# Performance work log

Measured on AMD Instinct MI355X. Metric: run time of the kernel, lower is better.

Reference implementation:

```python
import jax, jax.numpy as jnp
import numpy as np
from jax import lax

TAU = 2.0
V_TH = 1.0
ALPHA = 4.0   # spikingjelly surrogate.Sigmoid default
BN_EPS = 1e-5
HEADS = 8


def lif(x):
    """Multi-step LIF neuron (tau=2, v_reset=0, hard reset, detach_reset).
    x: [T, ...] -> spikes [T, ...]. Forward is Heaviside; sigmoid surrogate
    is wired in via straight-through for the bwd variant."""
    def step(v, xt):
        v = v + (xt - v) / TAU                      # charge
        sg = jax.nn.sigmoid(ALPHA * (v - V_TH))     # surrogate
        hard = (v >= V_TH).astype(x.dtype)
        spike = sg + lax.stop_gradient(hard - sg)   # fwd: hard, bwd: sigmoid'
        v = v * (1.0 - lax.stop_gradient(spike))    # detached hard reset to 0
        return v, spike
    _, s = lax.scan(step, jnp.zeros_like(x[0]), x)
    return s


def conv1x1_bn(x, w, g, b, m, var, bias=None):
    # x: [N, C, H, W]; 1x1 conv == channel matmul, then eval-mode BN
    y = jnp.einsum('nchw,dc->ndhw', x, w)
    if bias is not None:
        y = y + bias[None, :, None, None]
    scale = g / jnp.sqrt(var + BN_EPS)
    shift = b - m * scale
    return y * scale[None, :, None, None] + shift[None, :, None, None]


def to_heads(x, T, B, C, H, W):
    # [T,B,C,H,W] -> [T,B,heads,N,hd]
    N = H * W
    hd = C // HEADS
    x = x.reshape(T, B, C, N).transpose(0, 1, 3, 2)          # [T,B,N,C]
    return x.reshape(T, B, N, HEADS, hd).transpose(0, 1, 3, 2, 4)


def _forward(x, q_w, q_bn_g, q_bn_b, q_bn_m, q_bn_v,
             k_w, k_bn_g, k_bn_b, k_bn_m, k_bn_v,
             v_w, v_bn_g, v_bn_b, v_bn_m, v_bn_v,
             out_w, out_b, out_bn_g, out_bn_b, out_bn_m, out_bn_v):
    T, B, C, H, W = x.shape
    N = H * W
    identity = x

    xs = lif(x)                                  # shortcut_lif
    x_qkv = xs.reshape(T * B, C, H, W)

    q = lif(conv1x1_bn(x_qkv, q_w, q_bn_g, q_bn_b, q_bn_m, q_bn_v).reshape(T, B, C, H, W))
    k = lif(conv1x1_bn(x_qkv, k_w, k_bn_g, k_bn_b, k_bn_m, k_bn_v).reshape(T, B, C, H, W))
    v = lif(conv1x1_bn(x_qkv, v_w, v_bn_g, v_bn_b, v_bn_m, v_bn_v).reshape(T, B, C, H, W))

    qh = to_heads(q, T, B, C, H, W)              # [T,B,h,N,hd]
    kh = to_heads(k, T, B, C, H, W)
    vh = to_heads(v, T, B, C, H, W)

    kv = jnp.sum(kh * vh, axis=-2, keepdims=True)   # [T,B,h,1,hd]
    kv = lif(kv)                                    # talking_heads_proj_lif
    y = qh * kv                                     # [T,B,h,N,hd]

    # [T,B,h,N,hd] -> transpose(3,4) -> [T,B,h,hd,N] -> [T,B,C,H,W]
    y = y.transpose(0, 1, 2, 4, 3).reshape(T, B, C, H, W)
    y = conv1x1_bn(y.reshape(T * B, C, H, W), out_w, out_bn_g, out_bn_b,
                   out_bn_m, out_bn_v, bias=out_b).reshape(T, B, C, H, W)
    return y + identity, vh


def setup_inputs() -> dict:
    key = jax.random.key(0)
    ks = jax.random.split(key, 6)
    T, B, C, H, W = 4, 32, 512, 14, 14
    inp = {
        'x': jax.random.normal(ks[0], (T, B, C, H, W), dtype=jnp.float32),
        'q_w': jax.random.normal(ks[1], (C, C), dtype=jnp.float32) * 0.05,
        'k_w': jax.random.normal(ks[2], (C, C), dtype=jnp.float32) * 0.05,
        'v_w': jax.random.normal(ks[3], (C, C), dtype=jnp.float32) * 0.05,
        'out_w': jax.random.normal(ks[4], (C, C), dtype=jnp.float32) * 0.05,
        'out_b': jnp.zeros((C,), dtype=jnp.float32),
    }
    for p in ('q', 'k', 'v', 'out'):
        inp[f'{p}_bn_g'] = jnp.ones((C,), dtype=jnp.float32)
        inp[f'{p}_bn_b'] = jnp.zeros((C,), dtype=jnp.float32)
        inp[f'{p}_bn_m'] = jnp.zeros((C,), dtype=jnp.float32)
        inp[f'{p}_bn_v'] = jnp.ones((C,), dtype=jnp.float32)
    return inp


def reference(x, q_w, q_bn_g, q_bn_b, q_bn_m, q_bn_v,
              k_w, k_bn_g, k_bn_b, k_bn_m, k_bn_v,
              v_w, v_bn_g, v_bn_b, v_bn_m, v_bn_v,
              out_w, out_b, out_bn_g, out_bn_b, out_bn_m, out_bn_v):
    return _forward(x, q_w, q_bn_g, q_bn_b, q_bn_m, q_bn_v,
                    k_w, k_bn_g, k_bn_b, k_bn_m, k_bn_v,
                    v_w, v_bn_g, v_bn_b, v_bn_m, v_bn_v,
                    out_w, out_b, out_bn_g, out_bn_b, out_bn_m, out_bn_v)
```

## Files before the change

### kernel.cpp

```cpp
#include <hip/hip_runtime.h>
#include <math.h>

#define T_   4
#define B_   32
#define C_   512
#define N_   196
#define TB_  128
#define M_   25088
#define BNP_ 6272
#define OUT1_ 12845056

typedef unsigned short ushort_t;
typedef __attribute__((ext_vector_type(8)))  __bf16 bf16x8;
typedef __attribute__((ext_vector_type(16))) float  f32x16;

__device__ __forceinline__ ushort_t f2bf(float f) {
    unsigned int u = __float_as_uint(f);
    u = u + 0x7FFFu + ((u >> 16) & 1u);
    return (ushort_t)(u >> 16);
}
__device__ __forceinline__ float bf2f(ushort_t h) {
    return __uint_as_float(((unsigned int)h) << 16);
}

#define GL2LDS(gp, lp) \
    __builtin_amdgcn_global_load_lds((const __attribute__((address_space(1))) void*)(gp), \
                                     (__attribute__((address_space(3))) void*)(lp), 16, 0, 0)

__global__ __launch_bounds__(256)
void prep_lifx_kernel(
    const float* __restrict__ qw, const float* __restrict__ kw,
    const float* __restrict__ vw, const float* __restrict__ ow,
    const float* __restrict__ qg, const float* __restrict__ qb, const float* __restrict__ qm, const float* __restrict__ qv,
    const float* __restrict__ kg, const float* __restrict__ kb, const float* __restrict__ km, const float* __restrict__ kvr,
    const float* __restrict__ vg, const float* __restrict__ vb, const float* __restrict__ vm, const float* __restrict__ vv,
    const float* __restrict__ og, const float* __restrict__ ob, const float* __restrict__ om, const float* __restrict__ ov,
    const float* __restrict__ obias,
    ushort_t* __restrict__ wsplit, ushort_t* __restrict__ osplit,
    float* __restrict__ scale_qkv, float* __restrict__ shift_qkv,
    float* __restrict__ scale_o,   float* __restrict__ shift_o,
    float* __restrict__ kvpart,
    const float* __restrict__ x, ushort_t* __restrict__ xs)
{
    __shared__ ushort_t tile[64 * 66];
    const int bid = blockIdx.x;
    const int tid = threadIdx.x;

    if (bid < 3072) {
        int i = bid * 256 + tid;
        int d = i >> 9, c = i & 511;
        const float* src = (d < 512) ? qw : (d < 1024) ? kw : vw;
        float wv = src[(d & 511) * 512 + c];
        ushort_t h = f2bf(wv);
        float r1 = wv - bf2f(h);
        ushort_t mm = f2bf(r1);
        wsplit[((size_t)d * 2 + 0) * 512 + c] = h;
        wsplit[((size_t)d * 2 + 1) * 512 + c] = mm;
        if (d < 512)
            osplit[(size_t)d * 512 + c] = f2bf(ow[d * 512 + c]);

        if (i < 3 * C_) {
            int p = i >> 9, dl = i & 511;
            const float* g = (p == 0) ? qg : (p == 1) ? kg : vg;
            const float* b = (p == 0) ? qb : (p == 1) ? kb : vb;
            const float* m = (p == 0) ? qm : (p == 1) ? km : vm;
            const float* r = (p == 0) ? qv : (p == 1) ? kvr : vv;
            float sc = g[dl] / sqrtf(r[dl] + 1e-5f);
            scale_qkv[i] = sc;
            shift_qkv[i] = b[dl] - m[dl] * sc;
        }
        if (i < C_) {
            float sc = og[i] / sqrtf(ov[i] + 1e-5f);
            scale_o[i] = sc;
            shift_o[i] = ob[i] - om[i] * sc + obias[i] * sc;
        }
        if (i < TB_ * C_) kvpart[i] = 0.f;
        return;
    }

    const int l = bid - 3072;
    const int n0 = (l & 3) * 64;
    const int c0 = ((l >> 2) & 7) * 64;
    const int b  = l >> 5;
    const int j = tid & 63, w = tid >> 6;
    const bool nok = (n0 + j) < N_;
    float v[16];
#pragma unroll
    for (int r = 0; r < 16; ++r) v[r] = 0.f;
    for (int t = 0; t < T_; ++t) {
        const float* xb = x + ((size_t)((t * B_ + b) * C_ + c0)) * N_ + n0 + j;
#pragma unroll
        for (int r = 0; r < 16; ++r) {
            int i = w * 16 + r;
            float xv = nok ? xb[(size_t)i * N_] : 0.f;
            v[r] = v[r] + (xv - v[r]) * 0.5f;
            bool s = (v[r] >= 1.0f);
            tile[j * 66 + i] = s ? 0x3F80 : 0;
            if (s) v[r] = 0.f;
        }
        __syncthreads();
#pragma unroll
        for (int p = 0; p < 2; ++p) {
            int w2 = tid + p * 256;
            int jj = w2 >> 3, ck = w2 & 7;
            if (n0 + jj < N_) {
                const unsigned int* src = reinterpret_cast<const unsigned int*>(&tile[jj * 66 + ck * 8]);
                uint4 dv; dv.x = src[0]; dv.y = src[1]; dv.z = src[2]; dv.w = src[3];
                size_t mp = (size_t)(b * N_ + n0 + jj) * 4 + t;
                *reinterpret_cast<uint4*>(&xs[mp * 512 + c0 + ck * 8]) = dv;
            }
        }
        __syncthreads();
    }
}

__global__ __launch_bounds__(512, 4)
void qkv_gemm_lif(const ushort_t* __restrict__ W, const ushort_t* __restrict__ X,
                  const float* __restrict__ scale, const float* __restrict__ shift,
                  ushort_t* __restrict__ spk, float* __restrict__ out2)
{
    const int id = blockIdx.x;
    const int xw = id & 7, local = id >> 3;
    const int ml = local / 12, d_t = local - ml * 12;
    const int m_t = ml * 8 + xw;
    if (m_t >= 98) return;
    const int m0 = m_t * 256;
    const int d0 = d_t * 128;

    __shared__ ushort_t Xs[2][16 * 512];
    __shared__ ushort_t Ws[2][16 * 512];
    const int tid = threadIdx.x, wid = tid >> 6, lane = tid & 63;
    const int mw = (wid & 3) * 64, dw = (wid >> 2) * 64;
    const int row32 = lane & 31, khalf = lane >> 5;

    f32x16 acc[2][2] = {};

    auto STAGE = [&](int buf, int k0) {
        {
            int q = wid, mb = q >> 1, ks = q & 1;
            const ushort_t* g = X + (size_t)(m0 + mb * 32 + row32) * 512 + k0 + ks * 16 + khalf * 8;
            GL2LDS(g, &Xs[buf][q * 512]);
        }
        {
            int q = wid + 8, mb = q >> 1, ks = q & 1;
            const ushort_t* g = X + (size_t)(m0 + mb * 32 + row32) * 512 + k0 + ks * 16 + khalf * 8;
            GL2LDS(g, &Xs[buf][q * 512]);
        }
        {
            int q = wid, s = q >> 3, rem = q & 7, db = rem >> 1, ks = rem & 1;
            const ushort_t* g = W + ((size_t)(d0 + db * 32 + row32) * 2 + s) * 512 + k0 + ks * 16 + khalf * 8;
            GL2LDS(g, &Ws[buf][q * 512]);
        }
        {
            int q = wid + 8, s = q >> 3, rem = q & 7, db = rem >> 1, ks = rem & 1;
            const ushort_t* g = W + ((size_t)(d0 + db * 32 + row32) * 2 + s) * 512 + k0 + ks * 16 + khalf * 8;
            GL2LDS(g, &Ws[buf][q * 512]);
        }
    };

    STAGE(0, 0);
    __syncthreads();
    int cur = 0;

    for (int it = 0; it < 16; ++it) {
        if (it < 15) STAGE(cur ^ 1, (it + 1) * 32);

        __builtin_amdgcn_s_setprio(1);
#pragma unroll
        for (int ks = 0; ks < 2; ++ks) {
            bf16x8 xfr[2];
#pragma unroll
            for (int i = 0; i < 2; ++i)
                xfr[i] = *reinterpret_cast<const bf16x8*>(
                    &Xs[cur][(((mw >> 5) + i) * 2 + ks) * 512 + lane * 8]);
#pragma unroll
            for (int s = 0; s < 2; ++s)
#pragma unroll
                for (int j = 0; j < 2; ++j) {
                    bf16x8 wfr = *reinterpret_cast<const bf16x8*>(
                        &Ws[cur][(s * 8 + ((dw >> 5) + j) * 2 + ks) * 512 + lane * 8]);
#pragma unroll
                    for (int i = 0; i < 2; ++i)
                        acc[i][j] = __builtin_amdgcn_mfma_f32_32x32x16_bf16(xfr[i], wfr, acc[i][j], 0, 0, 0);
                }
        }
        __builtin_amdgcn_s_setprio(0);

        __syncthreads();
        cur ^= 1;
    }

    const int p = d0 >> 9;
    const bool isV = (p == 2);
    ushort_t* plane = spk + (size_t)p * ((size_t)M_ * 512);
#pragma unroll
    for (int j = 0; j < 2; ++j) {
        int d = d0 + dw + j * 32 + row32;
        float sc = scale[d], sh = shift[d];
        int dl = d & 511;
        int h = dl >> 6, hd = dl & 63;
#pragma unroll
        for (int i = 0; i < 2; ++i) {
            int bnb = (m0 + mw + i * 32) >> 2;
            f32x16 a = acc[i][j];
#pragma unroll
            for (int g = 0; g < 4; ++g) {
                int bn = bnb + 2 * g + khalf;
                float p0 = fmaf(a[4 * g + 0], sc, sh);
                float p1 = fmaf(a[4 * g + 1], sc, sh);
                float p2 = fmaf(a[4 * g + 2], sc, sh);
                float p3 = fmaf(a[4 * g + 3], sc, sh);
                float v = p0 * 0.5f;
                bool s0 = (v >= 1.f); if (s0) v = 0.f;
                v = v + (p1 - v) * 0.5f;
                bool s1 = (v >= 1.f); if (s1) v = 0.f;
                v = v + (p2 - v) * 0.5f;
                bool s2 = (v >= 1.f); if (s2) v = 0.f;
                v = v + (p3 - v) * 0.5f;
                bool s3 = (v >= 1.f);
                ushort_t* b0 = plane + (size_t)bn * 512 + dl;
                b0[0]                      = s0 ? 0x3F80 : 0;
                b0[(size_t)BNP_ * 512]     = s1 ? 0x3F80 : 0;
                b0[(size_t)2 * BNP_ * 512] = s2 ? 0x3F80 : 0;
                b0[(size_t)3 * BNP_ * 512] = s3 ? 0x3F80 : 0;
                if (isV) {
                    int b = bn / N_, n = bn - b * N_;
                    float* o = out2 + (((size_t)b * 8 + h) * N_ + n) * 64 + hd;
                    o[0]                       = s0 ? 1.f : 0.f;
                    o[(size_t)1 * (OUT1_ / 4)] = s1 ? 1.f : 0.f;
                    o[(size_t)2 * (OUT1_ / 4)] = s2 ? 1.f : 0.f;
                    o[(size_t)3 * (OUT1_ / 4)] = s3 ? 1.f : 0.f;
                }
            }
        }
    }
}

__global__ __launch_bounds__(256)
void kv_part_kernel(const ushort_t* __restrict__ ks, const ushort_t* __restrict__ vs,
                    float* __restrict__ kvpart)
{
    __shared__ int cnt[256];
    const int tid = threadIdx.x;
    cnt[tid] = 0;
    __syncthreads();
    const int tb = blockIdx.x >> 1, ch = blockIdx.x & 1;
    const int cg = tid & 31, ns = tid >> 5;
    const int c = ch * 256 + cg * 8;
    const ushort_t* kb = ks + (size_t)tb * N_ * 512 + c;
    const ushort_t* vb = vs + (size_t)tb * N_ * 512 + c;
    int loc[8] = {0, 0, 0, 0, 0, 0, 0, 0};
    int n1 = ns * 25 + 25; if (n1 > N_) n1 = N_;
    for (int n = ns * 25; n < n1; ++n) {
        uint4 kq = *reinterpret_cast<const uint4*>(&kb[(size_t)n * 512]);
        uint4 vq = *reinterpret_cast<const uint4*>(&vb[(size_t)n * 512]);
        unsigned m;
        m = kq.x & vq.x; loc[0] += (m & 0xFFFFu) ? 1 : 0; loc[1] += (m >> 16) ? 1 : 0;
        m = kq.y & vq.y; loc[2] += (m & 0xFFFFu) ? 1 : 0; loc[3] += (m >> 16) ? 1 : 0;
        m = kq.z & vq.z; loc[4] += (m & 0xFFFFu) ? 1 : 0; loc[5] += (m >> 16) ? 1 : 0;
        m = kq.w & vq.w; loc[6] += (m & 0xFFFFu) ? 1 : 0; loc[7] += (m >> 16) ? 1 : 0;
    }
#pragma unroll
    for (int e = 0; e < 8; ++e) atomicAdd(&cnt[cg * 8 + e], loc[e]);
    __syncthreads();
    kvpart[tb * 512 + ch * 256 + tid] = (float)cnt[tid];
}

__global__ void kv_lif_kernel(const float* __restrict__ kvpart, ushort_t* __restrict__ kvs)
{
    int i = blockIdx.x * 256 + threadIdx.x;
    if (i >= B_ * C_) return;
    int b = i >> 9, c = i & 511;
    float v = 0.f;
#pragma unroll
    for (int t = 0; t < T_; ++t) {
        float y = kvpart[((t * B_ + b) << 9) + c];
        v = v + (y - v) * 0.5f;
        bool s = (v >= 1.f);
        kvs[((t * B_ + b) << 9) + c] = s ? 0x3F80 : 0;
        if (s) v = 0.f;
    }
}

__global__ __launch_bounds__(256)
void out_gemm(const ushort_t* __restrict__ A, const ushort_t* __restrict__ qs,
              const ushort_t* __restrict__ kvs,
              const float* __restrict__ scale, const float* __restrict__ shift,
              const float* __restrict__ xid, float* __restrict__ out)
{
    const int id = blockIdx.x;
    const int xw = id & 7, local = id >> 3;
    const int m_t = (local >> 2) * 8 + xw, d_t = local & 3;
    if (m_t >= 196) return;
    const int m0 = m_t * 128, d0 = d_t * 128;

    __shared__ ushort_t As[2][8 * 512];
    __shared__ ushort_t Bs[2][8 * 512];
    const int tid = threadIdx.x, wid = tid >> 6, lane = tid & 63;
    const int dw = (wid >> 1) * 64, mw = (wid & 1) * 64;
    const int row32 = lane & 31, khalf = lane >> 5;

    int sm[2], stb[2], sq[2], sL[2];
#pragma unroll
    for (int u = 0; u < 2; ++u) {
        int s = tid + u * 256;
        sq[u] = s >> 6; sL[u] = s & 63;
        sm[u] = m0 + (sq[u] >> 1) * 32 + (sL[u] & 31);
        stb[u] = sm[u] / N_;
    }

    f32x16 acc[2][2] = {};

    {
        uint4 o[2];
#pragma unroll
        for (int u = 0; u < 2; ++u) {
            int kk = (sq[u] & 1) * 16 + (sL[u] >> 5) * 8;
            uint4 qv = *reinterpret_cast<const uint4*>(&qs[(size_t)sm[u] * 512 + kk]);
            uint4 kv = *reinterpret_cast<const uint4*>(&kvs[(size_t)stb[u] * 512 + kk]);
            o[u].x = qv.x & kv.x; o[u].y = qv.y & kv.y;
            o[u].z = qv.z & kv.z; o[u].w = qv.w & kv.w;
        }
        for (int q = wid; q < 8; q += 4) {
            int db = q >> 1, ks2 = q & 1;
            const ushort_t* g = A + (size_t)(d0 + db * 32 + row32) * 512 + ks2 * 16 + khalf * 8;
            GL2LDS(g, &As[0][q * 512]);
        }
#pragma unroll
        for (int u = 0; u < 2; ++u)
            *reinterpret_cast<uint4*>(&Bs[0][sq[u] * 512 + sL[u] * 8]) = o[u];
    }
    __syncthreads();

    int buf = 0;
    for (int it = 0; it < 16; ++it) {
        uint4 nq[2], nk[2];
        if (it < 15) {
            int k0n = (it + 1) * 32;
#pragma unroll
            for (int u = 0; u < 2; ++u) {
                int kk = k0n + (sq[u] & 1) * 16 + (sL[u] >> 5) * 8;
                nq[u] = *reinterpret_cast<const uint4*>(&qs[(size_t)sm[u] * 512 + kk]);
                nk[u] = *reinterpret_cast<const uint4*>(&kvs[(size_t)stb[u] * 512 + kk]);
            }
            for (int q = wid; q < 8; q += 4) {
                int db = q >> 1, ks2 = q & 1;
                const ushort_t* g = A + (size_t)(d0 + db * 32 + row32) * 512 + k0n + ks2 * 16 + khalf * 8;
                GL2LDS(g, &As[buf ^ 1][q * 512]);
            }
        }

        __builtin_amdgcn_s_setprio(1);
#pragma unroll
        for (int ks = 0; ks < 2; ++ks) {
            bf16x8 afr[2];
#pragma unroll
            for (int i = 0; i < 2; ++i)
                afr[i] = *reinterpret_cast<const bf16x8*>(
                    &As[buf][(((dw >> 5) + i) * 2 + ks) * 512 + lane * 8]);
#pragma unroll
            for (int j = 0; j < 2; ++j) {
                bf16x8 bfr = *reinterpret_cast<const bf16x8*>(
                    &Bs[buf][(((mw >> 5) + j) * 2 + ks) * 512 + lane * 8]);
#pragma unroll
                for (int i = 0; i < 2; ++i)
                    acc[i][j] = __builtin_amdgcn_mfma_f32_32x32x16_bf16(afr[i], bfr, acc[i][j], 0, 0, 0);
            }
        }
        __builtin_amdgcn_s_setprio(0);

        if (it < 15) {
#pragma unroll
            for (int u = 0; u < 2; ++u) {
                uint4 o;
                o.x = nq[u].x & nk[u].x; o.y = nq[u].y & nk[u].y;
                o.z = nq[u].z & nk[u].z; o.w = nq[u].w & nk[u].w;
                *reinterpret_cast<uint4*>(&Bs[buf ^ 1][sq[u] * 512 + sL[u] * 8]) = o;
            }
        }
        __syncthreads();
        buf ^= 1;
    }

#pragma unroll
    for (int j = 0; j < 2; ++j) {
        int m = m0 + mw + j * 32 + row32;
        int tb = m / N_;
        int n  = m - tb * N_;
        size_t mbase = (size_t)tb * (C_ * N_) + n;
#pragma unroll
        for (int i = 0; i < 2; ++i) {
            int dbase = d0 + dw + i * 32 + 4 * khalf;
            f32x16 a = acc[i][j];
#pragma unroll
            for (int g = 0; g < 4; ++g) {
#pragma unroll
                for (int t = 0; t < 4; ++t) {
                    int d = dbase + t + 8 * g;
                    float val = fmaf(a[4 * g + t], scale[d], shift[d]);
                    size_t ad = mbase + (size_t)d * N_;
                    out[ad] = val + xid[ad];
                }
            }
        }
    }
}

extern "C" void kernel_launch(void* const* d_in, const int* in_sizes, int n_in,
                              void* d_out, int out_size, void* d_ws, size_t ws_size,
                              hipStream_t stream)
{
    const float* x    = (const float*)d_in[0];
    const float* q_w  = (const float*)d_in[1];
    const float* k_w  = (const float*)d_in[2];
    const float* v_w  = (const float*)d_in[3];
    const float* o_w  = (const float*)d_in[4];
    const float* o_b  = (const float*)d_in[5];
    const float* qg = (const float*)d_in[6],  *qb = (const float*)d_in[7],
               *qm = (const float*)d_in[8],  *qv = (const float*)d_in[9];
    const float* kg = (const float*)d_in[10], *kb = (const float*)d_in[11],
               *km = (const float*)d_in[12], *kv = (const float*)d_in[13];
    const float* vg = (const float*)d_in[14], *vb = (const float*)d_in[15],
               *vm = (const float*)d_in[16], *vv = (const float*)d_in[17];
    const float* og = (const float*)d_in[18], *ob = (const float*)d_in[19],
               *om = (const float*)d_in[20], *ov = (const float*)d_in[21];

    float* out1  = (float*)d_out;
    float* out2f = out1 + OUT1_;

    ushort_t* spk    = (ushort_t*)d_ws;
    ushort_t* xs     = spk + (size_t)3 * M_ * 512;
    ushort_t* wsplit = xs + (size_t)M_ * 512;
    ushort_t* osplit = wsplit + (size_t)1536 * 2 * 512;
    float*    kvpart = (float*)(osplit + (size_t)512 * 512);
    ushort_t* kvs    = (ushort_t*)(kvpart + TB_ * C_);
    float*    scq    = (float*)(kvs + TB_ * C_);
    float*    shq    = scq + 3 * C_;
    float*    sco    = shq + 3 * C_;
    float*    sho    = sco + C_;

    ushort_t* qsp = spk;
    ushort_t* ksp = spk + (size_t)M_ * 512;
    ushort_t* vsp = spk + (size_t)2 * M_ * 512;

    prep_lifx_kernel<<<4096, 256, 0, stream>>>(
        q_w, k_w, v_w, o_w,
        qg, qb, qm, qv, kg, kb, km, kv, vg, vb, vm, vv, og, ob, om, ov, o_b,
        wsplit, osplit, scq, shq, sco, sho, kvpart, x, xs);

    qkv_gemm_lif<<<1200, 512, 0, stream>>>(wsplit, xs, scq, shq, spk, out2f);

    kv_part_kernel<<<256, 256, 0, stream>>>(ksp, vsp, kvpart);

    kv_lif_kernel<<<64, 256, 0, stream>>>(kvpart, kvs);

    out_gemm<<<800, 256, 0, stream>>>(osplit, qsp, kvs, sco, sho, x, out1);
}
```

Before: 404.0 us.

## Fuse K·V spike counting into QKV GEMM epilogue, skip K/V spike stores

Each block now computes Q, K and V for one M/channel tile sequentially. The K spikes are kept as ballot bitmasks in shared memory, and the V epilogue ANDs them with V spikes and accumulates per-batch counts into kvpart through LDS and global atomics. This removes the kv_part_kernel launch and the global writes and reads of the K and V spike planes. In exchange the grid shrinks from 1200 to 392 blocks, each doing three times the GEMM work, which lowers parallelism and occupancy. It also adds float atomics and relies on kvpart being zeroed by the prep kernel.

```diff
diff --git a/kernel.cpp b/kernel.cpp
--- a/kernel.cpp
+++ b/kernel.cpp
@@ -117,153 +117,173 @@
 __global__ __launch_bounds__(512, 4)
 void qkv_gemm_lif(const ushort_t* __restrict__ W, const ushort_t* __restrict__ X,
                   const float* __restrict__ scale, const float* __restrict__ shift,
-                  ushort_t* __restrict__ spk, float* __restrict__ out2)
+                  ushort_t* __restrict__ qspk, float* __restrict__ out2,
+                  float* __restrict__ kvpart)
 {
     const int id = blockIdx.x;
-    const int xw = id & 7, local = id >> 3;
-    const int ml = local / 12, d_t = local - ml * 12;
-    const int m_t = ml * 8 + xw;
-    if (m_t >= 98) return;
+    const int xcd = id & 7, local = id >> 3;
+    const int g = xcd * 49 + local;
+    const int m_t = g >> 2, d_t = g & 3;
     const int m0 = m_t * 256;
-    const int d0 = d_t * 128;
+    const int dl0 = d_t * 128;
 
     __shared__ ushort_t Xs[2][16 * 512];
     __shared__ ushort_t Ws[2][16 * 512];
+    __shared__ unsigned kmask[1024];
+    __shared__ int      cnt[1024];
+
     const int tid = threadIdx.x, wid = tid >> 6, lane = tid & 63;
     const int mw = (wid & 3) * 64, dw = (wid >> 2) * 64;
     const int row32 = lane & 31, khalf = lane >> 5;
 
-    f32x16 acc[2][2] = {};
-
-    auto STAGE = [&](int buf, int k0) {
-        {
-            int q = wid, mb = q >> 1, ks = q & 1;
-            const ushort_t* g = X + (size_t)(m0 + mb * 32 + row32) * 512 + k0 + ks * 16 + khalf * 8;
-            GL2LDS(g, &Xs[buf][q * 512]);
-        }
-        {
-            int q = wid + 8, mb = q >> 1, ks = q & 1;
-            const ushort_t* g = X + (size_t)(m0 + mb * 32 + row32) * 512 + k0 + ks * 16 + khalf * 8;
-            GL2LDS(g, &Xs[buf][q * 512]);
-        }
-        {
-            int q = wid, s = q >> 3, rem = q & 7, db = rem >> 1, ks = rem & 1;
-            const ushort_t* g = W + ((size_t)(d0 + db * 32 + row32) * 2 + s) * 512 + k0 + ks * 16 + khalf * 8;
-            GL2LDS(g, &Ws[buf][q * 512]);
-        }
-        {
-            int q = wid + 8, s = q >> 3, rem = q & 7, db = rem >> 1, ks = rem & 1;
-            const ushort_t* g = W + ((size_t)(d0 + db * 32 + row32) * 2 + s) * 512 + k0 + ks * 16 + khalf * 8;
-            GL2LDS(g, &Ws[buf][q * 512]);
+    const int bn0 = m_t * 64;
+    const int b0 = bn0 / N_;
+    const int bsplit = (b0 + 1) * N_ - bn0;
+
+    auto STAGE = [&](int buf, int k0, int d0g) {
+        {   int q = wid, mb = q >> 1, ks = q & 1;
+            const ushort_t* gp = X + (size_t)(m0 + mb * 32 + row32) * 512 + k0 + ks * 16 + khalf * 8;
+            GL2LDS(gp, &Xs[buf][q * 512]);
+        }
+        {   int q = wid + 8, mb = q >> 1, ks = q & 1;
+            const ushort_t* gp = X + (size_t)(m0 + mb * 32 + row32) * 512 + k0 + ks * 16 + khalf * 8;
+            GL2LDS(gp, &Xs[buf][q * 512]);
+        }
+        {   int q = wid, s = q >> 3, rem = q & 7, db = rem >> 1, ks = rem & 1;
+            const ushort_t* gp = W + ((size_t)(d0g + db * 32 + row32) * 2 + s) * 512 + k0 + ks * 16 + khalf * 8;
+            GL2LDS(gp, &Ws[buf][q * 512]);
+        }
+        {   int q = wid + 8, s = q >> 3, rem = q & 7, db = rem >> 1, ks = rem & 1;
+            const ushort_t* gp = W + ((size_t)(d0g + db * 32 + row32) * 2 + s) * 512 + k0 + ks * 16 + khalf * 8;
+            GL2LDS(gp, &Ws[buf][q * 512]);
         }
     };
 
-    STAGE(0, 0);
-    __syncthreads();
-    int cur = 0;
-
-    for (int it = 0; it < 16; ++it) {
-        if (it < 15) STAGE(cur ^ 1, (it + 1) * 32);
-
-        __builtin_amdgcn_s_setprio(1);
-#pragma unroll
-        for (int ks = 0; ks < 2; ++ks) {
-            bf16x8 xfr[2];
-#pragma unroll
-            for (int i = 0; i < 2; ++i)
-                xfr[i] = *reinterpret_cast<const bf16x8*>(
-                    &Xs[cur][(((mw >> 5) + i) * 2 + ks) * 512 + lane * 8]);
-#pragma unroll
-            for (int s = 0; s < 2; ++s)
-#pragma unroll
-                for (int j = 0; j < 2; ++j) {
-                    bf16x8 wfr = *reinterpret_cast<const bf16x8*>(
-                        &Ws[cur][(s * 8 + ((dw >> 5) + j) * 2 + ks) * 512 + lane * 8]);
-#pragma unroll
-                    for (int i = 0; i < 2; ++i)
-                        acc[i][j] = __builtin_amdgcn_mfma_f32_32x32x16_bf16(xfr[i], wfr, acc[i][j], 0, 0, 0);
+    for (int p = 0; p < 3; ++p) {
+        const int d0g = p * 512 + dl0;
+        f32x16 acc[2][2] = {};
+
+        STAGE(0, 0, d0g);
+        __syncthreads();
+        int cur = 0;
+        for (int it = 0; it < 16; ++it) {
+            if (it < 15) STAGE(cur ^ 1, (it + 1) * 32, d0g);
+
+            __builtin_amdgcn_s_setprio(1);
+#pragma unroll
+            for (int ks = 0; ks < 2; ++ks) {
+                bf16x8 xfr[2];
+#pragma unroll
+                for (int i = 0; i < 2; ++i)
+                    xfr[i] = *reinterpret_cast<const bf16x8*>(
+                        &Xs[cur][(((mw >> 5) + i) * 2 + ks) * 512 + lane * 8]);
+#pragma unroll
+                for (int s = 0; s < 2; ++s)
+#pragma unroll
+                    for (int j = 0; j < 2; ++j) {
+                        bf16x8 wfr = *reinterpret_cast<const bf16x8*>(
+                            &Ws[cur][(s * 8 + ((dw >> 5) + j) * 2 + ks) * 512 + lane * 8]);
+#pragma unroll
+                        for (int i = 0; i < 2; ++i)
+                            acc[i][j] = __builtin_amdgcn_mfma_f32_32x32x16_bf16(xfr[i], wfr, acc[i][j], 0, 0, 0);
+                    }
+            }
+            __builtin_amdgcn_s_setprio(0);
+            __syncthreads();
+            cur ^= 1;
+        }
+
+        if (p == 2) {
+            for (int w = tid; w < 1024; w += 512) cnt[w] = 0;
+            __syncthreads();
+        }
+
+#pragma unroll
+        for (int j = 0; j < 2; ++j) {
+            const int dl = dw + j * 32 + row32;
+            const int d  = d0g + dl;
+            const float sc = scale[d], sh = shift[d];
+            const int c = dl0 + dl;
+            const int dlblk = (dw >> 5) + j;
+            int rsum[4][2] = {{0,0},{0,0},{0,0},{0,0}};
+#pragma unroll
+            for (int i = 0; i < 2; ++i) {
+                const int bnb = (m0 + mw + i * 32) >> 2;
+                f32x16 a = acc[i][j];
+#pragma unroll
+                for (int g4 = 0; g4 < 4; ++g4) {
+                    int bn = bnb + 2 * g4 + khalf;
+                    float p0 = fmaf(a[4 * g4 + 0], sc, sh);
+                    float p1 = fmaf(a[4 * g4 + 1], sc, sh);
+                    float p2 = fmaf(a[4 * g4 + 2], sc, sh);
+                    float p3 = fmaf(a[4 * g4 + 3], sc, sh);
+                    float vm = p0 * 0.5f;
+                    bool s0 = (vm >= 1.f); if (s0) vm = 0.f;
+                    vm = vm + (p1 - vm) * 0.5f;
+                    bool s1 = (vm >= 1.f); if (s1) vm = 0.f;
+                    vm = vm + (p2 - vm) * 0.5f;
+                    bool s2 = (vm >= 1.f); if (s2) vm = 0.f;
+                    vm = vm + (p3 - vm) * 0.5f;
+                    bool s3 = (vm >= 1.f);
+
+                    if (p == 0) {
+                        ushort_t* bp = qspk + (size_t)bn * 512 + c;
+                        bp[0]                      = s0 ? 0x3F80 : 0;
+                        bp[(size_t)BNP_ * 512]     = s1 ? 0x3F80 : 0;
+                        bp[(size_t)2 * BNP_ * 512] = s2 ? 0x3F80 : 0;
+                        bp[(size_t)3 * BNP_ * 512] = s3 ? 0x3F80 : 0;
+                    } else if (p == 1) {
+                        const int bnl_e = (bnb + 2 * g4) - bn0;
+                        const int widx = bnl_e * 16 + 0 * 4 + dlblk;
+                        bool sarr[4] = {s0, s1, s2, s3};
+#pragma unroll
+                        for (int t = 0; t < 4; ++t) {
+                            unsigned long long bm = __ballot(sarr[t]);
+                            if (lane == 0)
+                                kmask[widx + t * 4]      = (unsigned)bm;
+                            else if (lane == 32)
+                                kmask[widx + t * 4 + 16] = (unsigned)(bm >> 32);
+                        }
+                    } else {
+                        int b = bn / N_, n = bn - b * N_;
+                        float* o = out2 + (((size_t)b * 8 + (c >> 6)) * N_ + n) * 64 + (c & 63);
+                        o[0]                       = s0 ? 1.f : 0.f;
+                        o[(size_t)1 * (OUT1_ / 4)] = s1 ? 1.f : 0.f;
+                        o[(size_t)2 * (OUT1_ / 4)] = s2 ? 1.f : 0.f;
+                        o[(size_t)3 * (OUT1_ / 4)] = s3 ? 1.f : 0.f;
+                        const int bnl = bn - bn0;
+                        const int slot = (bnl >= bsplit) ? 1 : 0;
+                        bool sarr[4] = {s0, s1, s2, s3};
+#pragma unroll
+                        for (int t = 0; t < 4; ++t) {
+                            unsigned kw_ = kmask[bnl * 16 + t * 4 + dlblk];
+                            rsum[t][slot] += (int)((kw_ >> row32) & 1u) & (sarr[t] ? 1 : 0);
+                        }
+                    }
                 }
-        }
-        __builtin_amdgcn_s_setprio(0);
-
+            }
+            if (p == 2) {
+#pragma unroll
+                for (int t = 0; t < 4; ++t) {
+                    if (rsum[t][0]) atomicAdd(&cnt[t * 256 + 0 + dl], rsum[t][0]);
+                    if (rsum[t][1]) atomicAdd(&cnt[t * 256 + 128 + dl], rsum[t][1]);
+                }
+            }
+        }
+
+        if (p == 2) {
+            __syncthreads();
+            for (int w = tid; w < 1024; w += 512) {
+                int val = cnt[w];
+                if (val) {
+                    int t = w >> 8, slot = (w >> 7) & 1, dl = w & 127;
+                    int b = b0 + slot;
+                    atomicAdd(&kvpart[(t * 32 + b) * 512 + dl0 + dl], (float)val);
+                }
+            }
+        }
         __syncthreads();
-        cur ^= 1;
-    }
-
-    const int p = d0 >> 9;
-    const bool isV = (p == 2);
-    ushort_t* plane = spk + (size_t)p * ((size_t)M_ * 512);
-#pragma unroll
-    for (int j = 0; j < 2; ++j) {
-        int d = d0 + dw + j * 32 + row32;
-        float sc = scale[d], sh = shift[d];
-        int dl = d & 511;
-        int h = dl >> 6, hd = dl & 63;
-#pragma unroll
-        for (int i = 0; i < 2; ++i) {
-            int bnb = (m0 + mw + i * 32) >> 2;
-            f32x16 a = acc[i][j];
-#pragma unroll
-            for (int g = 0; g < 4; ++g) {
-                int bn = bnb + 2 * g + khalf;
-                float p0 = fmaf(a[4 * g + 0], sc, sh);
-                float p1 = fmaf(a[4 * g + 1], sc, sh);
-                float p2 = fmaf(a[4 * g + 2], sc, sh);
-                float p3 = fmaf(a[4 * g + 3], sc, sh);
-                float v = p0 * 0.5f;
-                bool s0 = (v >= 1.f); if (s0) v = 0.f;
-                v = v + (p1 - v) * 0.5f;
-                bool s1 = (v >= 1.f); if (s1) v = 0.f;
-                v = v + (p2 - v) * 0.5f;
-                bool s2 = (v >= 1.f); if (s2) v = 0.f;
-                v = v + (p3 - v) * 0.5f;
-                bool s3 = (v >= 1.f);
-                ushort_t* b0 = plane + (size_t)bn * 512 + dl;
-                b0[0]                      = s0 ? 0x3F80 : 0;
-                b0[(size_t)BNP_ * 512]     = s1 ? 0x3F80 : 0;
-                b0[(size_t)2 * BNP_ * 512] = s2 ? 0x3F80 : 0;
-                b0[(size_t)3 * BNP_ * 512] = s3 ? 0x3F80 : 0;
-                if (isV) {
-                    int b = bn / N_, n = bn - b * N_;
-                    float* o = out2 + (((size_t)b * 8 + h) * N_ + n) * 64 + hd;
-                    o[0]                       = s0 ? 1.f : 0.f;
-                    o[(size_t)1 * (OUT1_ / 4)] = s1 ? 1.f : 0.f;
-                    o[(size_t)2 * (OUT1_ / 4)] = s2 ? 1.f : 0.f;
-                    o[(size_t)3 * (OUT1_ / 4)] = s3 ? 1.f : 0.f;
-                }
-            }
-        }
-    }
-}
-
-__global__ __launch_bounds__(256)
-void kv_part_kernel(const ushort_t* __restrict__ ks, const ushort_t* __restrict__ vs,
-                    float* __restrict__ kvpart)
-{
-    __shared__ int cnt[256];
-    const int tid = threadIdx.x;
-    cnt[tid] = 0;
-    __syncthreads();
-    const int tb = blockIdx.x >> 1, ch = blockIdx.x & 1;
-    const int cg = tid & 31, ns = tid >> 5;
-    const int c = ch * 256 + cg * 8;
-    const ushort_t* kb = ks + (size_t)tb * N_ * 512 + c;
-    const ushort_t* vb = vs + (size_t)tb * N_ * 512 + c;
-    int loc[8] = {0, 0, 0, 0, 0, 0, 0, 0};
-    int n1 = ns * 25 + 25; if (n1 > N_) n1 = N_;
-    for (int n = ns * 25; n < n1; ++n) {
-        uint4 kq = *reinterpret_cast<const uint4*>(&kb[(size_t)n * 512]);
-        uint4 vq = *reinterpret_cast<const uint4*>(&vb[(size_t)n * 512]);
-        unsigned m;
-        m = kq.x & vq.x; loc[0] += (m & 0xFFFFu) ? 1 : 0; loc[1] += (m >> 16) ? 1 : 0;
-        m = kq.y & vq.y; loc[2] += (m & 0xFFFFu) ? 1 : 0; loc[3] += (m >> 16) ? 1 : 0;
-        m = kq.z & vq.z; loc[4] += (m & 0xFFFFu) ? 1 : 0; loc[5] += (m >> 16) ? 1 : 0;
-        m = kq.w & vq.w; loc[6] += (m & 0xFFFFu) ? 1 : 0; loc[7] += (m >> 16) ? 1 : 0;
-    }
-#pragma unroll
-    for (int e = 0; e < 8; ++e) atomicAdd(&cnt[cg * 8 + e], loc[e]);
-    __syncthreads();
-    kvpart[tb * 512 + ch * 256 + tid] = (float)cnt[tid];
+    }
 }
 
 __global__ void kv_lif_kernel(const float* __restrict__ kvpart, ushort_t* __restrict__ kvs)
@@ -440,17 +460,13 @@
     float*    sho    = sco + C_;
 
     ushort_t* qsp = spk;
-    ushort_t* ksp = spk + (size_t)M_ * 512;
-    ushort_t* vsp = spk + (size_t)2 * M_ * 512;
 
     prep_lifx_kernel<<<4096, 256, 0, stream>>>(
         q_w, k_w, v_w, o_w,
         qg, qb, qm, qv, kg, kb, km, kv, vg, vb, vm, vv, og, ob, om, ov, o_b,
         wsplit, osplit, scq, shq, sco, sho, kvpart, x, xs);
 
-    qkv_gemm_lif<<<1200, 512, 0, stream>>>(wsplit, xs, scq, shq, spk, out2f);
-
-    kv_part_kernel<<<256, 256, 0, stream>>>(ksp, vsp, kvpart);
+    qkv_gemm_lif<<<392, 512, 0, stream>>>(wsplit, xs, scq, shq, qsp, out2f, kvpart);
 
     kv_lif_kernel<<<64, 256, 0, stream>>>(kvpart, kvs);
 
```

Measured after the change: 627.1 us. 1.55x slower.

## Pack K/V spikes into ballot bitmasks and fuse kv reduction with LIF

Applied to the files above, without the earlier changes.

The QKV GEMM epilogue now writes K and V spikes as 32-bit bitmasks built with wave ballots, instead of full bf16 spike planes. Q spikes keep the old bf16 layout. The kv count reduction and the kv LIF kernel are merged into one kernel that ANDs the bitmask words and counts bits per channel. This removes most of the K/V spike write and read-back traffic and one kernel launch. In exchange, the fused kernel loops serially over all tokens per thread with low parallelism, which may be latency-bound.

```diff
diff --git a/kernel.cpp b/kernel.cpp
--- a/kernel.cpp
+++ b/kernel.cpp
@@ -117,7 +117,8 @@
 __global__ __launch_bounds__(512, 4)
 void qkv_gemm_lif(const ushort_t* __restrict__ W, const ushort_t* __restrict__ X,
                   const float* __restrict__ scale, const float* __restrict__ shift,
-                  ushort_t* __restrict__ spk, float* __restrict__ out2)
+                  ushort_t* __restrict__ qspk, float* __restrict__ out2,
+                  unsigned* __restrict__ kbit, unsigned* __restrict__ vbit)
 {
     const int id = blockIdx.x;
     const int xw = id & 7, local = id >> 3;
@@ -136,23 +137,19 @@
     f32x16 acc[2][2] = {};
 
     auto STAGE = [&](int buf, int k0) {
-        {
-            int q = wid, mb = q >> 1, ks = q & 1;
+        {   int q = wid, mb = q >> 1, ks = q & 1;
             const ushort_t* g = X + (size_t)(m0 + mb * 32 + row32) * 512 + k0 + ks * 16 + khalf * 8;
             GL2LDS(g, &Xs[buf][q * 512]);
         }
-        {
-            int q = wid + 8, mb = q >> 1, ks = q & 1;
+        {   int q = wid + 8, mb = q >> 1, ks = q & 1;
             const ushort_t* g = X + (size_t)(m0 + mb * 32 + row32) * 512 + k0 + ks * 16 + khalf * 8;
             GL2LDS(g, &Xs[buf][q * 512]);
         }
-        {
-            int q = wid, s = q >> 3, rem = q & 7, db = rem >> 1, ks = rem & 1;
+        {   int q = wid, s = q >> 3, rem = q & 7, db = rem >> 1, ks = rem & 1;
             const ushort_t* g = W + ((size_t)(d0 + db * 32 + row32) * 2 + s) * 512 + k0 + ks * 16 + khalf * 8;
             GL2LDS(g, &Ws[buf][q * 512]);
         }
-        {
-            int q = wid + 8, s = q >> 3, rem = q & 7, db = rem >> 1, ks = rem & 1;
+        {   int q = wid + 8, s = q >> 3, rem = q & 7, db = rem >> 1, ks = rem & 1;
             const ushort_t* g = W + ((size_t)(d0 + db * 32 + row32) * 2 + s) * 512 + k0 + ks * 16 + khalf * 8;
             GL2LDS(g, &Ws[buf][q * 512]);
         }
@@ -185,20 +182,20 @@
                 }
         }
         __builtin_amdgcn_s_setprio(0);
-
         __syncthreads();
         cur ^= 1;
     }
 
     const int p = d0 >> 9;
-    const bool isV = (p == 2);
-    ushort_t* plane = spk + (size_t)p * ((size_t)M_ * 512);
+    const bool isQ = (p == 0), isV = (p == 2);
+    unsigned* __restrict__ bitp = (p == 1) ? kbit : vbit;
 #pragma unroll
     for (int j = 0; j < 2; ++j) {
         int d = d0 + dw + j * 32 + row32;
         float sc = scale[d], sh = shift[d];
         int dl = d & 511;
         int h = dl >> 6, hd = dl & 63;
+        int cw = ((d0 & 511) + dw + j * 32) >> 5;
 #pragma unroll
         for (int i = 0; i < 2; ++i) {
             int bnb = (m0 + mw + i * 32) >> 2;
@@ -218,18 +215,32 @@
                 bool s2 = (v >= 1.f); if (s2) v = 0.f;
                 v = v + (p3 - v) * 0.5f;
                 bool s3 = (v >= 1.f);
-                ushort_t* b0 = plane + (size_t)bn * 512 + dl;
-                b0[0]                      = s0 ? 0x3F80 : 0;
-                b0[(size_t)BNP_ * 512]     = s1 ? 0x3F80 : 0;
-                b0[(size_t)2 * BNP_ * 512] = s2 ? 0x3F80 : 0;
-                b0[(size_t)3 * BNP_ * 512] = s3 ? 0x3F80 : 0;
-                if (isV) {
-                    int b = bn / N_, n = bn - b * N_;
-                    float* o = out2 + (((size_t)b * 8 + h) * N_ + n) * 64 + hd;
-                    o[0]                       = s0 ? 1.f : 0.f;
-                    o[(size_t)1 * (OUT1_ / 4)] = s1 ? 1.f : 0.f;
-                    o[(size_t)2 * (OUT1_ / 4)] = s2 ? 1.f : 0.f;
-                    o[(size_t)3 * (OUT1_ / 4)] = s3 ? 1.f : 0.f;
+
+                if (isQ) {
+                    ushort_t* b0 = qspk + (size_t)bn * 512 + dl;
+                    b0[0]                      = s0 ? 0x3F80 : 0;
+                    b0[(size_t)BNP_ * 512]     = s1 ? 0x3F80 : 0;
+                    b0[(size_t)2 * BNP_ * 512] = s2 ? 0x3F80 : 0;
+                    b0[(size_t)3 * BNP_ * 512] = s3 ? 0x3F80 : 0;
+                } else {
+                    const int bn_e = bnb + 2 * g;
+                    bool sarr[4] = {s0, s1, s2, s3};
+#pragma unroll
+                    for (int t = 0; t < 4; ++t) {
+                        unsigned long long bm = __ballot(sarr[t]);
+                        if (lane == 0)
+                            bitp[((size_t)t * BNP_ + bn_e) * 16 + cw] = (unsigned)bm;
+                        else if (lane == 32)
+                            bitp[((size_t)t * BNP_ + bn_e + 1) * 16 + cw] = (unsigned)(bm >> 32);
+                    }
+                    if (isV) {
+                        int b = bn / N_, n = bn - b * N_;
+                        float* o = out2 + (((size_t)b * 8 + h) * N_ + n) * 64 + hd;
+                        o[0]                       = s0 ? 1.f : 0.f;
+                        o[(size_t)1 * (OUT1_ / 4)] = s1 ? 1.f : 0.f;
+                        o[(size_t)2 * (OUT1_ / 4)] = s2 ? 1.f : 0.f;
+                        o[(size_t)3 * (OUT1_ / 4)] = s3 ? 1.f : 0.f;
+                    }
                 }
             }
         }
@@ -237,44 +248,24 @@
 }
 
 __global__ __launch_bounds__(256)
-void kv_part_kernel(const ushort_t* __restrict__ ks, const ushort_t* __restrict__ vs,
-                    float* __restrict__ kvpart)
+void kv_bit_lif(const unsigned* __restrict__ kbit, const unsigned* __restrict__ vbit,
+                ushort_t* __restrict__ kvs)
 {
-    __shared__ int cnt[256];
-    const int tid = threadIdx.x;
-    cnt[tid] = 0;
-    __syncthreads();
-    const int tb = blockIdx.x >> 1, ch = blockIdx.x & 1;
-    const int cg = tid & 31, ns = tid >> 5;
-    const int c = ch * 256 + cg * 8;
-    const ushort_t* kb = ks + (size_t)tb * N_ * 512 + c;
-    const ushort_t* vb = vs + (size_t)tb * N_ * 512 + c;
-    int loc[8] = {0, 0, 0, 0, 0, 0, 0, 0};
-    int n1 = ns * 25 + 25; if (n1 > N_) n1 = N_;
-    for (int n = ns * 25; n < n1; ++n) {
-        uint4 kq = *reinterpret_cast<const uint4*>(&kb[(size_t)n * 512]);
-        uint4 vq = *reinterpret_cast<const uint4*>(&vb[(size_t)n * 512]);
-        unsigned m;
-        m = kq.x & vq.x; loc[0] += (m & 0xFFFFu) ? 1 : 0; loc[1] += (m >> 16) ? 1 : 0;
-        m = kq.y & vq.y; loc[2] += (m & 0xFFFFu) ? 1 : 0; loc[3] += (m >> 16) ? 1 : 0;
-        m = kq.z & vq.z; loc[4] += (m & 0xFFFFu) ? 1 : 0; loc[5] += (m >> 16) ? 1 : 0;
-        m = kq.w & vq.w; loc[6] += (m & 0xFFFFu) ? 1 : 0; loc[7] += (m >> 16) ? 1 : 0;
-    }
-#pragma unroll
-    for (int e = 0; e < 8; ++e) atomicAdd(&cnt[cg * 8 + e], loc[e]);
-    __syncthreads();
-    kvpart[tb * 512 + ch * 256 + tid] = (float)cnt[tid];
-}
-
-__global__ void kv_lif_kernel(const float* __restrict__ kvpart, ushort_t* __restrict__ kvs)
-{
-    int i = blockIdx.x * 256 + threadIdx.x;
-    if (i >= B_ * C_) return;
-    int b = i >> 9, c = i & 511;
+    int id = blockIdx.x * 256 + threadIdx.x;
+    if (id >= B_ * C_) return;
+    int b = id >> 9, c = id & 511;
+    int cw = c >> 5, bit = c & 31;
     float v = 0.f;
 #pragma unroll
     for (int t = 0; t < T_; ++t) {
-        float y = kvpart[((t * B_ + b) << 9) + c];
+        size_t base = ((size_t)t * BNP_ + (size_t)b * N_) * 16 + cw;
+        int cnt = 0;
+        for (int n = 0; n < N_; ++n) {
+            unsigned kw = kbit[base + (size_t)n * 16];
+            unsigned vw = vbit[base + (size_t)n * 16];
+            cnt += (int)(((kw & vw) >> bit) & 1u);
+        }
+        float y = (float)cnt;
         v = v + (y - v) * 0.5f;
         bool s = (v >= 1.f);
         kvs[((t * B_ + b) << 9) + c] = s ? 0x3F80 : 0;
@@ -440,19 +431,17 @@
     float*    sho    = sco + C_;
 
     ushort_t* qsp = spk;
-    ushort_t* ksp = spk + (size_t)M_ * 512;
-    ushort_t* vsp = spk + (size_t)2 * M_ * 512;
+    unsigned* kbit = (unsigned*)(spk + (size_t)M_ * 512);
+    unsigned* vbit = (unsigned*)(spk + (size_t)2 * M_ * 512);
 
     prep_lifx_kernel<<<4096, 256, 0, stream>>>(
         q_w, k_w, v_w, o_w,
         qg, qb, qm, qv, kg, kb, km, kv, vg, vb, vm, vv, og, ob, om, ov, o_b,
         wsplit, osplit, scq, shq, sco, sho, kvpart, x, xs);
 
-    qkv_gemm_lif<<<1200, 512, 0, stream>>>(wsplit, xs, scq, shq, spk, out2f);
-
-    kv_part_kernel<<<256, 256, 0, stream>>>(ksp, vsp, kvpart);
-
-    kv_lif_kernel<<<64, 256, 0, stream>>>(kvpart, kvs);
+    qkv_gemm_lif<<<1200, 512, 0, stream>>>(wsplit, xs, scq, shq, qsp, out2f, kbit, vbit);
+
+    kv_bit_lif<<<64, 256, 0, stream>>>(kbit, vbit, kvs);
 
     out_gemm<<<800, 256, 0, stream>>>(osplit, qsp, kvs, sco, sho, x, out1);
 }
```

Result: slower. 476.9 us (+18.0%).
